# Optimization experiments

Hardware: AMD Instinct MI355X
Metric: run time of the kernel (lower is better)

The kernel has to match this reference:

```python
import jax, jax.numpy as jnp
import numpy as np
from jax import lax

B, T, D, H, L = 2048, 512, 64, 16, 10
LOG2PI = float(np.log(2.0 * np.pi))


def _gru_cell(x, h, Wih, Whh, bih, bhh):
    # torch GRUCell gate order: r, z, n
    gi = x @ Wih.T + bih
    gh = h @ Whh.T + bhh
    ir, iz, inn = jnp.split(gi, 3, axis=-1)
    hr, hz, hn = jnp.split(gh, 3, axis=-1)
    r = jax.nn.sigmoid(ir + hr)
    z = jax.nn.sigmoid(iz + hz)
    n = jnp.tanh(inn + r * hn)
    return (1.0 - z) * n + z * h


def _mlp_head(h, W1, b1, W2, b2, Wmu, bmu, Wcov, bcov):
    hh = jax.nn.relu(h @ W1.T + b1)
    hh = jax.nn.relu(hh @ W2.T + b2)
    mu = hh @ Wmu.T + bmu
    sigma = jnp.exp(hh @ Wcov.T + bcov)
    return mu, sigma


def setup_inputs():
    key = jax.random.key(0)
    ks = jax.random.split(key, 24)

    def he(k, shape, fan_in):
        return jax.random.normal(k, shape, dtype=jnp.float32) * np.float32(np.sqrt(2.0 / fan_in))

    z = lambda *s: jnp.zeros(s, jnp.float32)
    p = {}
    p['x'] = jax.random.normal(ks[0], (B, T, D), dtype=jnp.float32)
    p['eps'] = jax.random.normal(ks[1], (B, T, L), dtype=jnp.float32)
    # bidirectional inference GRU
    p['bi_Wih_f'] = he(ks[2], (3 * H, D), D); p['bi_Whh_f'] = he(ks[3], (3 * H, H), H)
    p['bi_bih_f'] = z(3 * H); p['bi_bhh_f'] = z(3 * H)
    p['bi_Wih_b'] = he(ks[4], (3 * H, D), D); p['bi_Whh_b'] = he(ks[5], (3 * H, H), H)
    p['bi_bih_b'] = z(3 * H); p['bi_bhh_b'] = z(3 * H)
    # inference GRUCell on [z_prev, context]
    p['infz_Wih'] = he(ks[6], (3 * H, L + 2 * H), L + 2 * H); p['infz_Whh'] = he(ks[7], (3 * H, H), H)
    p['infz_bih'] = z(3 * H); p['infz_bhh'] = z(3 * H)
    # inference MLP
    p['inf_W1'] = he(ks[8], (H, H), H); p['inf_b1'] = z(H)
    p['inf_W2'] = he(ks[9], (H, H), H); p['inf_b2'] = z(H)
    p['inf_Wmu'] = he(ks[10], (L, H), H); p['inf_bmu'] = z(L)
    p['inf_Wcov'] = he(ks[11], (L, H), H); p['inf_bcov'] = z(L)
    # generative prior GRUCell + MLP (frozen in torch)
    p['genz_Wih'] = he(ks[12], (3 * H, L), L); p['genz_Whh'] = he(ks[13], (3 * H, H), H)
    p['genz_bih'] = z(3 * H); p['genz_bhh'] = z(3 * H)
    p['genzmlp_W1'] = he(ks[14], (H, H), H); p['genzmlp_b1'] = z(H)
    p['genzmlp_W2'] = he(ks[15], (H, H), H); p['genzmlp_b2'] = z(H)
    p['genzmlp_Wmu'] = he(ks[16], (L, H), H); p['genzmlp_bmu'] = z(L)
    p['genzmlp_Wcov'] = he(ks[17], (L, H), H); p['genzmlp_bcov'] = z(L)
    # generative emission GRUCell + MLP (outputs 3*D)
    p['genr_Wih'] = he(ks[18], (3 * H, L), L); p['genr_Whh'] = he(ks[19], (3 * H, H), H)
    p['genr_bih'] = z(3 * H); p['genr_bhh'] = z(3 * H)
    p['genr_W1'] = he(ks[20], (H, H), H); p['genr_b1'] = z(H)
    p['genr_W2'] = he(ks[21], (3 * D, H), H); p['genr_b2'] = z(3 * D)
    return p


def _forward(x, eps, bi_Wih_f, bi_Whh_f, bi_bih_f, bi_bhh_f, bi_Wih_b, bi_Whh_b, bi_bih_b, bi_bhh_b,
             infz_Wih, infz_Whh, infz_bih, infz_bhh,
             inf_W1, inf_b1, inf_W2, inf_b2, inf_Wmu, inf_bmu, inf_Wcov, inf_bcov,
             genz_Wih, genz_Whh, genz_bih, genz_bhh,
             genzmlp_W1, genzmlp_b1, genzmlp_W2, genzmlp_b2, genzmlp_Wmu, genzmlp_bmu, genzmlp_Wcov, genzmlp_bcov,
             genr_Wih, genr_Whh, genr_bih, genr_bhh, genr_W1, genr_b1, genr_W2, genr_b2):
    b, t, d = x.shape
    xt = jnp.transpose(x, (1, 0, 2))      # [T, B, D] time-major
    eps_t = jnp.transpose(eps, (1, 0, 2))  # [T, B, L]
    h0 = jnp.zeros((b, H), x.dtype)

    def fstep(h, xin):
        h2 = _gru_cell(xin, h, bi_Wih_f, bi_Whh_f, bi_bih_f, bi_bhh_f)
        return h2, h2

    def bstep(h, xin):
        h2 = _gru_cell(xin, h, bi_Wih_b, bi_Whh_b, bi_bih_b, bi_bhh_b)
        return h2, h2

    _, fwd = lax.scan(fstep, h0, xt)               # [T, B, H]
    _, bwd_rev = lax.scan(bstep, h0, xt[::-1])
    bwd = bwd_rev[::-1]                            # [T, B, H]

    pad = jnp.zeros((1, b, H), x.dtype)
    h_right = jnp.concatenate([pad, fwd[:-1]], axis=0)   # h^{->}_{t-1}
    h_left = jnp.concatenate([bwd[1:], pad], axis=0)     # h^{<-}_{t+1}
    ctx = jnp.concatenate([h_right, h_left], axis=-1)    # [T, B, 2H]

    def step(carry, inp):
        h_z, h_gz, h_gr, z_prev = carry
        c, e, xi = inp
        h_z = _gru_cell(jnp.concatenate([z_prev, c], axis=-1), h_z, infz_Wih, infz_Whh, infz_bih, infz_bhh)
        q_mu, q_sig = _mlp_head(h_z, inf_W1, inf_b1, inf_W2, inf_b2, inf_Wmu, inf_bmu, inf_Wcov, inf_bcov)
        h_gz = _gru_cell(z_prev, h_gz, genz_Wih, genz_Whh, genz_bih, genz_bhh)
        p_mu, p_sig = _mlp_head(h_gz, genzmlp_W1, genzmlp_b1, genzmlp_W2, genzmlp_b2, genzmlp_Wmu, genzmlp_bmu, genzmlp_Wcov, genzmlp_bcov)
        # KL(N(q_mu,q_sig) || N(p_mu,p_sig))
        kl = jnp.log(p_sig / q_sig) + (q_sig * q_sig + (q_mu - p_mu) ** 2) / (2.0 * p_sig * p_sig) - 0.5
        kl_t = kl.sum(axis=-1).mean()
        z_t = q_mu + q_sig * e  # rsample
        h_gr = _gru_cell(z_t, h_gr, genr_Wih, genr_Whh, genr_bih, genr_bhh)
        r = jax.nn.relu(h_gr @ genr_W1.T + genr_b1) @ genr_W2.T + genr_b2  # [B, 3D]
        r_mu = r[:, :d]
        r_diag = jnp.exp(r[:, d:2 * d]) + 1e-4
        w = r[:, 2 * d:]  # rank-1 cov factor
        # LowRankMVN log_prob via Woodbury (rank 1): Cov = D + w w^T
        delta = xi - r_mu
        dinv = 1.0 / r_diag
        wd = w * dinv
        cap = 1.0 + jnp.sum(wd * w, axis=-1)  # capacitance
        maha = jnp.sum(delta * delta * dinv, axis=-1) - jnp.sum(wd * delta, axis=-1) ** 2 / cap
        logdet = jnp.sum(jnp.log(r_diag), axis=-1) + jnp.log(cap)
        logp = -0.5 * (d * LOG2PI + logdet + maha)
        nll_t = -logp.mean()
        return (h_z, h_gz, h_gr, z_t), (kl_t, nll_t)

    z0 = jnp.zeros((b, L), x.dtype)
    carry0 = (h0, h0, h0, z0)
    _, (kls, nlls) = lax.scan(step, carry0, (ctx, eps_t, xt))
    return nlls.sum(), kls.sum()


def reference(x, eps, bi_Wih_f, bi_Whh_f, bi_bih_f, bi_bhh_f, bi_Wih_b, bi_Whh_b, bi_bih_b, bi_bhh_b,
              infz_Wih, infz_Whh, infz_bih, infz_bhh,
              inf_W1, inf_b1, inf_W2, inf_b2, inf_Wmu, inf_bmu, inf_Wcov, inf_bcov,
              genz_Wih, genz_Whh, genz_bih, genz_bhh,
              genzmlp_W1, genzmlp_b1, genzmlp_W2, genzmlp_b2, genzmlp_Wmu, genzmlp_bmu, genzmlp_Wcov, genzmlp_bcov,
              genr_Wih, genr_Whh, genr_bih, genr_bhh, genr_W1, genr_b1, genr_W2, genr_b2):
    return _forward(x, eps, bi_Wih_f, bi_Whh_f, bi_bih_f, bi_bhh_f, bi_Wih_b, bi_Whh_b, bi_bih_b, bi_bhh_b,
                    infz_Wih, infz_Whh, infz_bih, infz_bhh,
                    inf_W1, inf_b1, inf_W2, inf_b2, inf_Wmu, inf_bmu, inf_Wcov, inf_bcov,
                    genz_Wih, genz_Whh, genz_bih, genz_bhh,
                    genzmlp_W1, genzmlp_b1, genzmlp_W2, genzmlp_b2, genzmlp_Wmu, genzmlp_bmu, genzmlp_Wcov, genzmlp_bcov,
                    genr_Wih, genr_Whh, genr_bih, genr_bhh, genr_W1, genr_b1, genr_W2, genr_b2)
```

## Files before the change

kernel.cpp:

```cpp
#include <hip/hip_runtime.h>

namespace {

typedef __attribute__((ext_vector_type(4))) _Float16 half4v;
typedef __attribute__((ext_vector_type(4))) float   float4v;
typedef unsigned int u32;

#define MFMA16(a,b,c) __builtin_amdgcn_mfma_f32_16x16x16f16((a),(b),(c),0,0,0)

constexpr int Bb = 2048;
constexpr int Tt = 512;
constexpr float LOG2PI_ = 1.8378770664093453f;

struct InPtrs { const float* p[42]; };

__device__ __forceinline__ float rcpf(float x){ return __builtin_amdgcn_rcpf(x); }
__device__ __forceinline__ float sigm(float x){ return rcpf(1.0f + __expf(-x)); }
__device__ __forceinline__ float tanh_(float x){ return 1.0f - 2.0f*rcpf(1.0f + __expf(2.0f*x)); }

__device__ __forceinline__ void barrier_lds(){
  asm volatile("s_waitcnt lgkmcnt(0)" ::: "memory");
  __builtin_amdgcn_s_barrier();
  asm volatile("" ::: "memory");
}

__global__ void zero2(float* out){ if (threadIdx.x < 2) out[threadIdx.x] = 0.f; }

__device__ __forceinline__ void gru_update(const float4v& Dr, const float4v& Dz,
                                           const float4v& Dn, const float4v& Dh, half4v& hB){
  #pragma unroll
  for (int i = 0; i < 4; ++i){
    const float rr = sigm(Dr[i]);
    const float zz = sigm(Dz[i]);
    const float nn = tanh_(Dn[i] + rr*Dh[i]);
    const float hp = (float)hB[i];
    hB[i] = (_Float16)(nn + zz*(hp - nn));
  }
}

__device__ __forceinline__ half4v relu_pack(const float4v& D){
  half4v o;
  #pragma unroll
  for (int i = 0; i < 4; ++i) o[i] = (_Float16)fmaxf(D[i], 0.f);
  return o;
}

constexpr int CH = 8;
constexpr int NCH = Tt / CH;

__global__ __launch_bounds__(128,1) void bigru(InPtrs ip, _Float16* __restrict__ hf,
                                               _Float16* __restrict__ hb)
{
  const int tid = threadIdx.x;
  const int w = tid >> 6;
  const int l = tid & 63, r = l & 15, q = l >> 4;
  const int dir = blockIdx.y;
  const int base = blockIdx.x * 16;

  const float* __restrict__ x   = ip.p[0];
  const float* __restrict__ Wih = dir ? ip.p[6] : ip.p[2];
  const float* __restrict__ Whh = dir ? ip.p[7] : ip.p[3];
  const float* __restrict__ bih = dir ? ip.p[8] : ip.p[4];
  const float* __restrict__ bhh = dir ? ip.p[9] : ip.p[5];
  _Float16* __restrict__ hout = dir ? hb : hf;

  __shared__ __align__(16) float giS[2][CH][64][12];

  half4v Wi[3][4];
  float  b0[4], b1[4], b2[4];
  float4v xp[CH][4];
  half4v Wh[3];
  float  bh2[4];
  half4v hB = {0,0,0,0};
  const float* xrow = x + (size_t)(base + r) * Tt * 64;

  if (w == 1){
    #pragma unroll
    for (int rt = 0; rt < 3; ++rt)
      #pragma unroll
      for (int kt = 0; kt < 4; ++kt)
        #pragma unroll
        for (int j = 0; j < 4; ++j)
          Wi[rt][kt][j] = (_Float16)Wih[(rt*16 + r)*64 + kt*16 + q*4 + j];
    #pragma unroll
    for (int i = 0; i < 4; ++i){
      const int row = q*4 + i;
      b0[i] = bih[row]      + bhh[row];
      b1[i] = bih[16 + row] + bhh[16 + row];
      b2[i] = bih[32 + row];
    }
    #pragma unroll
    for (int s = 0; s < CH; ++s){
      const int tn = dir ? Tt-1-s : s;
      #pragma unroll
      for (int kt = 0; kt < 4; ++kt)
        xp[s][kt] = *(const float4v*)(xrow + (size_t)tn*64 + kt*16 + q*4);
    }
  } else {
    #pragma unroll
    for (int rt = 0; rt < 3; ++rt)
      #pragma unroll
      for (int j = 0; j < 4; ++j)
        Wh[rt][j] = (_Float16)Whh[(rt*16 + r)*16 + q*4 + j];
    #pragma unroll
    for (int i = 0; i < 4; ++i) bh2[i] = bhh[32 + q*4 + i];
  }

  for (int c = 0; c < NCH; ++c){
    if (w == 1){
      #pragma unroll
      for (int st = 0; st < CH; ++st){
        const int tg = c*CH + st;
        half4v xB[4];
        #pragma unroll
        for (int kt = 0; kt < 4; ++kt)
          #pragma unroll
          for (int j = 0; j < 4; ++j) xB[kt][j] = (_Float16)xp[st][kt][j];
        const int tp = tg + CH;
        if (tp < Tt){
          const int tn = dir ? Tt-1-tp : tp;
          #pragma unroll
          for (int kt = 0; kt < 4; ++kt)
            xp[st][kt] = *(const float4v*)(xrow + (size_t)tn*64 + kt*16 + q*4);
        }
        float4v A0 = {b0[0],b0[1],b0[2],b0[3]};
        float4v A1 = {b1[0],b1[1],b1[2],b1[3]};
        float4v A2 = {b2[0],b2[1],b2[2],b2[3]};
        #pragma unroll
        for (int kt = 0; kt < 4; ++kt){
          A0 = MFMA16(Wi[0][kt], xB[kt], A0);
          A1 = MFMA16(Wi[1][kt], xB[kt], A1);
          A2 = MFMA16(Wi[2][kt], xB[kt], A2);
        }
        float* o = &giS[c&1][st][l][0];
        *(float4v*)(o + 0) = A0;
        *(float4v*)(o + 4) = A1;
        *(float4v*)(o + 8) = A2;
      }
    }
    barrier_lds();
    if (w == 0){
      #pragma unroll
      for (int st = 0; st < CH; ++st){
        const int tg = c*CH + st;
        const int t = dir ? Tt-1-tg : tg;
        const float* gi = &giS[c&1][st][l][0];
        float4v A0 = *(const float4v*)(gi + 0);
        float4v A1 = *(const float4v*)(gi + 4);
        float4v A2 = *(const float4v*)(gi + 8);
        float4v Dh = {bh2[0],bh2[1],bh2[2],bh2[3]};
        A0 = MFMA16(Wh[0], hB, A0);
        A1 = MFMA16(Wh[1], hB, A1);
        Dh = MFMA16(Wh[2], hB, Dh);
        gru_update(A0, A1, A2, Dh, hB);
        *(half4v*)(hout + (((size_t)t*Bb + base + r) << 4) + q*4) = hB;
      }
    }
  }
}

__global__ __launch_bounds__(192,1) void vae_seq(InPtrs ip, const _Float16* __restrict__ hf,
                                                 const _Float16* __restrict__ hb,
                                                 _Float16* __restrict__ hz,
                                                 _Float16* __restrict__ hgz,
                                                 _Float16* __restrict__ hgr)
{
  const int tid = threadIdx.x;
  const int w = tid / 64;
  const int l = tid & 63, r = l & 15, q = l >> 4;
  const int base = blockIdx.x * 16;
  const int row0 = q*4;

  __shared__ u32 zS[3][2][64];
  for (int i = tid; i < 3*2*64; i += 192) ((u32*)zS)[i] = 0u;
  barrier_lds();

  half4v WizA[3][3], WhzA[3], I1A, I2A, IMuA, ICovA;
  float bz0[4], bz1[4], bzn[4], bzh[4], bI1v[4], bI2v[4], bIMu[4], bICov[4];
  half4v hzB = {0,0,0,0}, zB = {0,0,0,0};
  half4v hrR[4], hlR[4];
  float4v eR[4];
  half4v WgzA[3], WhgzA[3];
  float bg0[4], bg1[4], bgn[4], bgh[4];
  half4v hgzB = {0,0,0,0};
  half4v WgrA[3], WhgrA[3];
  float br0[4], br1[4], brn[4], brh[4];
  half4v hgrB = {0,0,0,0};

  const float* erow = ip.p[1] + (size_t)(base + r) * Tt * 10;

  if (w == 0){
    #pragma unroll
    for (int rt = 0; rt < 3; ++rt)
      #pragma unroll
      for (int kt = 0; kt < 3; ++kt)
        #pragma unroll
        for (int j = 0; j < 4; ++j){
          const int k = kt*16 + q*4 + j;
          int c;
          if (kt == 0) c = (k < 10) ? k : -1;
          else if (kt == 1) c = 10 + (k - 16);
          else c = 26 + (k - 32);
          WizA[rt][kt][j] = (c >= 0) ? (_Float16)ip.p[10][(rt*16 + r)*42 + c] : (_Float16)0.f;
        }
    #pragma unroll
    for (int rt = 0; rt < 3; ++rt)
      #pragma unroll
      for (int j = 0; j < 4; ++j)
        WhzA[rt][j] = (_Float16)ip.p[11][(rt*16 + r)*16 + q*4 + j];
    #pragma unroll
    for (int j = 0; j < 4; ++j){
      const int k = q*4 + j;
      I1A[j]  = (_Float16)ip.p[14][r*16 + k];
      I2A[j]  = (_Float16)ip.p[16][r*16 + k];
      IMuA[j] = (r < 10) ? (_Float16)ip.p[18][r*16 + k] : (_Float16)0.f;
      ICovA[j]= (r < 10) ? (_Float16)ip.p[20][r*16 + k] : (_Float16)0.f;
    }
    #pragma unroll
    for (int i = 0; i < 4; ++i){
      const int row = row0 + i;
      bz0[i] = ip.p[12][row]    + ip.p[13][row];
      bz1[i] = ip.p[12][16+row] + ip.p[13][16+row];
      bzn[i] = ip.p[12][32+row];
      bzh[i] = ip.p[13][32+row];
      bI1v[i] = ip.p[15][row];  bI2v[i] = ip.p[17][row];
      bIMu[i]  = (row < 10) ? ip.p[19][row] : 0.f;
      bICov[i] = (row < 10) ? ip.p[21][row] : 0.f;
    }
    #pragma unroll
    for (int s = 0; s < 4; ++s){
      if (s >= 1) hrR[s] = *(const half4v*)(hf + (((size_t)(s-1)*Bb + base + r) << 4) + q*4);
      else { half4v z0 = {0,0,0,0}; hrR[s] = z0; }
      hlR[s] = *(const half4v*)(hb + (((size_t)(s+1)*Bb + base + r) << 4) + q*4);
      float4v et;
      #pragma unroll
      for (int ii = 0; ii < 4; ++ii) et[ii] = (row0 + ii < 10) ? erow[s*10 + row0 + ii] : 0.f;
      eR[s] = et;
    }
  } else if (w == 1){
    #pragma unroll
    for (int rt = 0; rt < 3; ++rt)
      #pragma unroll
      for (int j = 0; j < 4; ++j){
        const int k = q*4 + j;
        WgzA[rt][j]  = (k < 10) ? (_Float16)ip.p[22][(rt*16 + r)*10 + k] : (_Float16)0.f;
        WhgzA[rt][j] = (_Float16)ip.p[23][(rt*16 + r)*16 + k];
      }
    #pragma unroll
    for (int i = 0; i < 4; ++i){
      const int row = row0 + i;
      bg0[i] = ip.p[24][row]    + ip.p[25][row];
      bg1[i] = ip.p[24][16+row] + ip.p[25][16+row];
      bgn[i] = ip.p[24][32+row];
      bgh[i] = ip.p[25][32+row];
    }
  } else {
    #pragma unroll
    for (int rt = 0; rt < 3; ++rt)
      #pragma unroll
      for (int j = 0; j < 4; ++j){
        const int k = q*4 + j;
        WgrA[rt][j]  = (k < 10) ? (_Float16)ip.p[34][(rt*16 + r)*10 + k] : (_Float16)0.f;
        WhgrA[rt][j] = (_Float16)ip.p[35][(rt*16 + r)*16 + k];
      }
    #pragma unroll
    for (int i = 0; i < 4; ++i){
      const int row = row0 + i;
      br0[i] = ip.p[36][row]    + ip.p[37][row];
      br1[i] = ip.p[36][16+row] + ip.p[37][16+row];
      brn[i] = ip.p[36][32+row];
      brh[i] = ip.p[37][32+row];
    }
  }

  for (int ib = 0; ib < Tt + 4; ib += 4){
    #pragma unroll
    for (int k = 0; k < 4; ++k){
      const int i = ib + k;
      if (w == 0){
        if (i < Tt){
          const half4v hrB = hrR[k], hlB = hlR[k];
          const float4v ev = eR[k];
          const int f = i + 4;
          if (f < Tt){
            hrR[k] = *(const half4v*)(hf + (((size_t)(f-1)*Bb + base + r) << 4) + q*4);
            if (f <= Tt-2) hlR[k] = *(const half4v*)(hb + (((size_t)(f+1)*Bb + base + r) << 4) + q*4);
            else { half4v z0 = {0,0,0,0}; hlR[k] = z0; }
            float4v et;
            #pragma unroll
            for (int ii = 0; ii < 4; ++ii) et[ii] = (row0 + ii < 10) ? erow[f*10 + row0 + ii] : 0.f;
            eR[k] = et;
          }
          float4v Dr = {bz0[0],bz0[1],bz0[2],bz0[3]};
          float4v Dz = {bz1[0],bz1[1],bz1[2],bz1[3]};
          float4v Dn = {bzn[0],bzn[1],bzn[2],bzn[3]};
          float4v Dh = {bzh[0],bzh[1],bzh[2],bzh[3]};
          Dr = MFMA16(WizA[0][1], hrB, Dr); Dr = MFMA16(WizA[0][2], hlB, Dr);
          Dz = MFMA16(WizA[1][1], hrB, Dz); Dz = MFMA16(WizA[1][2], hlB, Dz);
          Dn = MFMA16(WizA[2][1], hrB, Dn); Dn = MFMA16(WizA[2][2], hlB, Dn);
          Dr = MFMA16(WhzA[0], hzB, Dr);
          Dz = MFMA16(WhzA[1], hzB, Dz);
          Dh = MFMA16(WhzA[2], hzB, Dh);
          Dr = MFMA16(WizA[0][0], zB, Dr);
          Dz = MFMA16(WizA[1][0], zB, Dz);
          Dn = MFMA16(WizA[2][0], zB, Dn);
          gru_update(Dr, Dz, Dn, Dh, hzB);
          *(half4v*)(hz + (((size_t)i*Bb + base + r) << 4) + q*4) = hzB;

          float4v H1 = {bI1v[0],bI1v[1],bI1v[2],bI1v[3]};
          H1 = MFMA16(I1A, hzB, H1);
          const half4v h1B = relu_pack(H1);
          float4v H2 = {bI2v[0],bI2v[1],bI2v[2],bI2v[3]};
          H2 = MFMA16(I2A, h1B, H2);
          const half4v h2B = relu_pack(H2);
          float4v Qmu  = {bIMu[0],bIMu[1],bIMu[2],bIMu[3]};
          float4v Qpre = {bICov[0],bICov[1],bICov[2],bICov[3]};
          Qmu  = MFMA16(IMuA,  h2B, Qmu);
          Qpre = MFMA16(ICovA, h2B, Qpre);

          const int slot = i % 3;
          #pragma unroll
          for (int ii = 0; ii < 4; ++ii){
            const float qs = __expf(Qpre[ii]);
            zB[ii] = (_Float16)(Qmu[ii] + qs*ev[ii]);
          }
          union { half4v h; u32 u[2]; } zc; zc.h = zB;
          zS[slot][0][l] = zc.u[0];
          zS[slot][1][l] = zc.u[1];
        }
      } else if (w == 1){
        if (i >= 1 && i <= Tt){
          const int s = i - 1;
          const int sp = (s - 1 + 3) % 3;
          union { half4v h; u32 u[2]; } zc;
          zc.u[0] = zS[sp][0][l]; zc.u[1] = zS[sp][1][l];
          const half4v zPrev = zc.h;

          float4v Er = {bg0[0],bg0[1],bg0[2],bg0[3]};
          float4v Ez = {bg1[0],bg1[1],bg1[2],bg1[3]};
          float4v En = {bgn[0],bgn[1],bgn[2],bgn[3]};
          float4v Eh = {bgh[0],bgh[1],bgh[2],bgh[3]};
          Er = MFMA16(WgzA[0], zPrev, Er); Er = MFMA16(WhgzA[0], hgzB, Er);
          Ez = MFMA16(WgzA[1], zPrev, Ez); Ez = MFMA16(WhgzA[1], hgzB, Ez);
          En = MFMA16(WgzA[2], zPrev, En);
          Eh = MFMA16(WhgzA[2], hgzB, Eh);
          gru_update(Er, Ez, En, Eh, hgzB);
          *(half4v*)(hgz + (((size_t)s*Bb + base + r) << 4) + q*4) = hgzB;
        }
      } else {
        if (i >= 2 && i < Tt + 2){
          const int u = i - 2;
          union { half4v h; u32 uu[2]; } zc;
          zc.uu[0] = zS[u % 3][0][l]; zc.uu[1] = zS[u % 3][1][l];
          const half4v zU = zc.h;

          float4v Fr = {br0[0],br0[1],br0[2],br0[3]};
          float4v Fz = {br1[0],br1[1],br1[2],br1[3]};
          float4v Fn = {brn[0],brn[1],brn[2],brn[3]};
          float4v Fh = {brh[0],brh[1],brh[2],brh[3]};
          Fr = MFMA16(WgrA[0], zU, Fr); Fr = MFMA16(WhgrA[0], hgrB, Fr);
          Fz = MFMA16(WgrA[1], zU, Fz); Fz = MFMA16(WhgrA[1], hgrB, Fz);
          Fn = MFMA16(WgrA[2], zU, Fn);
          Fh = MFMA16(WhgrA[2], hgrB, Fh);
          gru_update(Fr, Fz, Fn, Fh, hgrB);
          *(half4v*)(hgr + (((size_t)u*Bb + base + r) << 4) + q*4) = hgrB;
        }
      }
      barrier_lds();
    }
  }
}

__global__ __launch_bounds__(256,2) void epi(InPtrs ip, const _Float16* __restrict__ hz,
                                             const _Float16* __restrict__ hgz,
                                             const _Float16* __restrict__ hgr,
                                             float* __restrict__ out)
{
  const int tid = threadIdx.x;
  const int l = tid & 63, r = l & 15, q = l >> 4;
  const int row0 = q*4;

  if (blockIdx.x < 1024){
    const int wid = blockIdx.x * 4 + (tid >> 6);
    const int u0 = wid * 16;

    half4v I1A, I2A, IMuA, ICovA, Z1A, Z2A, ZMuA, ZCovA;
    float bI1v[4], bI2v[4], bIMu[4], bICov[4], bZ1v[4], bZ2v[4], bZMu[4], bZCov[4];
    #pragma unroll
    for (int j = 0; j < 4; ++j){
      const int k = q*4 + j;
      I1A[j]  = (_Float16)ip.p[14][r*16 + k];
      I2A[j]  = (_Float16)ip.p[16][r*16 + k];
      IMuA[j] = (r < 10) ? (_Float16)ip.p[18][r*16 + k] : (_Float16)0.f;
      ICovA[j]= (r < 10) ? (_Float16)ip.p[20][r*16 + k] : (_Float16)0.f;
      Z1A[j]  = (_Float16)ip.p[26][r*16 + k];
      Z2A[j]  = (_Float16)ip.p[28][r*16 + k];
      ZMuA[j] = (r < 10) ? (_Float16)ip.p[30][r*16 + k] : (_Float16)0.f;
      ZCovA[j]= (r < 10) ? (_Float16)ip.p[32][r*16 + k] : (_Float16)0.f;
    }
    #pragma unroll
    for (int i = 0; i < 4; ++i){
      const int row = row0 + i;
      bI1v[i] = ip.p[15][row];  bI2v[i] = ip.p[17][row];
      bIMu[i]  = (row < 10) ? ip.p[19][row] : 0.f;
      bICov[i] = (row < 10) ? ip.p[21][row] : 0.f;
      bZ1v[i] = ip.p[27][row];  bZ2v[i] = ip.p[29][row];
      bZMu[i]  = (row < 10) ? ip.p[31][row] : 0.f;
      bZCov[i] = (row < 10) ? ip.p[33][row] : 0.f;
    }

    float kl_acc = 0.f;
    for (int k = 0; k < 16; ++k){
      const int u = u0 + k;
      const int tile = u >> 9, t = u & 511;
      const size_t off = (((size_t)t*Bb + tile*16 + r) << 4) + q*4;
      const half4v hzB  = *(const half4v*)(hz  + off);
      const half4v hgzB = *(const half4v*)(hgz + off);

      float4v H1 = {bI1v[0],bI1v[1],bI1v[2],bI1v[3]};
      H1 = MFMA16(I1A, hzB, H1);
      const half4v h1B = relu_pack(H1);
      float4v H2 = {bI2v[0],bI2v[1],bI2v[2],bI2v[3]};
      H2 = MFMA16(I2A, h1B, H2);
      const half4v h2B = relu_pack(H2);
      float4v Qmu  = {bIMu[0],bIMu[1],bIMu[2],bIMu[3]};
      float4v Qpre = {bICov[0],bICov[1],bICov[2],bICov[3]};
      Qmu  = MFMA16(IMuA,  h2B, Qmu);
      Qpre = MFMA16(ICovA, h2B, Qpre);

      float4v G1 = {bZ1v[0],bZ1v[1],bZ1v[2],bZ1v[3]};
      G1 = MFMA16(Z1A, hgzB, G1);
      const half4v g1B = relu_pack(G1);
      float4v G2 = {bZ2v[0],bZ2v[1],bZ2v[2],bZ2v[3]};
      G2 = MFMA16(Z2A, g1B, G2);
      const half4v g2B = relu_pack(G2);
      float4v Pmu  = {bZMu[0],bZMu[1],bZMu[2],bZMu[3]};
      float4v Ppre = {bZCov[0],bZCov[1],bZCov[2],bZCov[3]};
      Pmu  = MFMA16(ZMuA,  g2B, Pmu);
      Ppre = MFMA16(ZCovA, g2B, Ppre);

      #pragma unroll
      for (int ii = 0; ii < 4; ++ii){
        const float qs = __expf(Qpre[ii]);
        const float dm = Qmu[ii] - Pmu[ii];
        kl_acc += (Ppre[ii] - Qpre[ii]) + (qs*qs + dm*dm)*0.5f*__expf(-2.f*Ppre[ii]) - 0.5f;
      }
    }
    #pragma unroll
    for (int m = 1; m < 64; m <<= 1) kl_acc += __shfl_xor(kl_acc, m, 64);
    if (l == 0) atomicAdd(&out[1], kl_acc * (1.f/(float)Bb));
  } else {
    const int wid = (blockIdx.x - 1024) * 4 + (tid >> 6);
    const int u0 = wid * 16;

    half4v R1A, R2A[12];
    float bR1v[4], bR2v[12][4];
    #pragma unroll
    for (int j = 0; j < 4; ++j){
      const int k = q*4 + j;
      R1A[j] = (_Float16)ip.p[38][r*16 + k];
      #pragma unroll
      for (int m = 0; m < 12; ++m)
        R2A[m][j] = (_Float16)ip.p[40][(m*16 + r)*16 + k];
    }
    #pragma unroll
    for (int i = 0; i < 4; ++i){
      const int row = row0 + i;
      bR1v[i] = ip.p[39][row];
      #pragma unroll
      for (int m = 0; m < 12; ++m) bR2v[m][i] = ip.p[41][m*16 + row];
    }

    float nll_acc = 0.f;
    for (int k = 0; k < 16; ++k){
      const int u = u0 + k;
      const int tile = u >> 9, t = u & 511;
      const half4v hgrB = *(const half4v*)(hgr + (((size_t)t*Bb + tile*16 + r) << 4) + q*4);
      const float* xrow = ip.p[0] + ((size_t)(tile*16 + r) * Tt + t) * 64;
      float4v xv[4];
      #pragma unroll
      for (int m = 0; m < 4; ++m) xv[m] = *(const float4v*)(xrow + m*16 + q*4);

      float4v R1D = {bR1v[0],bR1v[1],bR1v[2],bR1v[3]};
      R1D = MFMA16(R1A, hgrB, R1D);
      const half4v r1B = relu_pack(R1D);

      float s1 = 0.f, s2 = 0.f, s3 = 0.f, s4 = 0.f;
      #pragma unroll
      for (int m = 0; m < 4; ++m){
        float4v Dmu = {bR2v[m][0],bR2v[m][1],bR2v[m][2],bR2v[m][3]};
        float4v Ddp = {bR2v[4+m][0],bR2v[4+m][1],bR2v[4+m][2],bR2v[4+m][3]};
        float4v Dw  = {bR2v[8+m][0],bR2v[8+m][1],bR2v[8+m][2],bR2v[8+m][3]};
        Dmu = MFMA16(R2A[m],   r1B, Dmu);
        Ddp = MFMA16(R2A[4+m], r1B, Ddp);
        Dw  = MFMA16(R2A[8+m], r1B, Dw);
        #pragma unroll
        for (int ii = 0; ii < 4; ++ii){
          const float diag = __expf(Ddp[ii]) + 1e-4f;
          const float dinv = rcpf(diag);
          const float delta = xv[m][ii] - Dmu[ii];
          const float wv = Dw[ii];
          s1 += delta*delta*dinv;
          s2 += wv*wv*dinv;
          s3 += wv*dinv*delta;
          s4 += __logf(diag);
        }
      }
      s1 += __shfl_xor(s1, 16, 64); s1 += __shfl_xor(s1, 32, 64);
      s2 += __shfl_xor(s2, 16, 64); s2 += __shfl_xor(s2, 32, 64);
      s3 += __shfl_xor(s3, 16, 64); s3 += __shfl_xor(s3, 32, 64);
      s4 += __shfl_xor(s4, 16, 64); s4 += __shfl_xor(s4, 32, 64);
      const float cap = 1.f + s2;
      const float maha = s1 - s3*s3*rcpf(cap);
      const float logdet = s4 + __logf(cap);
      nll_acc += 0.5f*(64.f*LOG2PI_ + logdet + maha);
    }
    #pragma unroll
    for (int m = 1; m < 64; m <<= 1) nll_acc += __shfl_xor(nll_acc, m, 64);
    if (l == 0) atomicAdd(&out[0], nll_acc * 0.25f * (1.f/(float)Bb));
  }
}

}

extern "C" void kernel_launch(void* const* d_in, const int* in_sizes, int n_in,
                              void* d_out, int out_size, void* d_ws, size_t ws_size,
                              hipStream_t stream)
{
  InPtrs ip;
  for (int i = 0; i < 42; ++i) ip.p[i] = (const float*)d_in[i];
  float* out = (float*)d_out;

  const size_t SZ = (size_t)Tt * Bb * 16;
  _Float16* hf  = (_Float16*)d_ws;
  _Float16* hb  = hf  + SZ;
  _Float16* hz  = hb  + SZ;
  _Float16* hgz = hz  + SZ;
  _Float16* hgr = hgz + SZ;

  zero2<<<1, 64, 0, stream>>>(out);
  dim3 gb(Bb/16, 2);
  bigru<<<gb, 128, 0, stream>>>(ip, hf, hb);
  vae_seq<<<Bb/16, 192, 0, stream>>>(ip, hf, hb, hz, hgz, hgr);
  epi<<<2048, 256, 0, stream>>>(ip, hz, hgz, hgr, out);
}
```

Before: 1.029 ms.

## Halve barriers in wavefront-pipelined VAE sequence via deeper z ring buffer

The z ring buffer shared between the three wave roles grows from 3 to 8 slots, and the downstream waves now lag by 2 and 4 steps instead of 1 and 2. This lets the loop skip the LDS barrier on every other iteration, cutting barrier stalls on the serial time loop. Separately, the float atomics into the output are replaced by per-block partial sums plus a final single-block reduction kernel, which also removes the zeroing kernel. The deeper lag adds a few pipeline drain steps, and correctness relies on the slot and lag arithmetic staying race-free with half the barriers.

Result: faster. 996.9 us (-3.1%).

```diff
diff --git a/kernel.cpp b/kernel.cpp
--- a/kernel.cpp
+++ b/kernel.cpp
@@ -23,8 +23,6 @@
   __builtin_amdgcn_s_barrier();
   asm volatile("" ::: "memory");
 }
-
-__global__ void zero2(float* out){ if (threadIdx.x < 2) out[threadIdx.x] = 0.f; }
 
 __device__ __forceinline__ void gru_update(const float4v& Dr, const float4v& Dz,
                                            const float4v& Dn, const float4v& Dh, half4v& hB){
@@ -171,8 +169,8 @@
   const int base = blockIdx.x * 16;
   const int row0 = q*4;
 
-  __shared__ u32 zS[3][2][64];
-  for (int i = tid; i < 3*2*64; i += 192) ((u32*)zS)[i] = 0u;
+  __shared__ u32 zS[8][2][64];
+  for (int i = tid; i < 8*2*64; i += 192) ((u32*)zS)[i] = 0u;
   barrier_lds();
 
   half4v WizA[3][3], WhzA[3], I1A, I2A, IMuA, ICovA;
@@ -318,21 +316,21 @@
           Qmu  = MFMA16(IMuA,  h2B, Qmu);
           Qpre = MFMA16(ICovA, h2B, Qpre);
 
-          const int slot = i % 3;
           #pragma unroll
           for (int ii = 0; ii < 4; ++ii){
             const float qs = __expf(Qpre[ii]);
             zB[ii] = (_Float16)(Qmu[ii] + qs*ev[ii]);
           }
           union { half4v h; u32 u[2]; } zc; zc.h = zB;
+          const int slot = i & 7;
           zS[slot][0][l] = zc.u[0];
           zS[slot][1][l] = zc.u[1];
         }
       } else if (w == 1){
-        if (i >= 1 && i <= Tt){
-          const int s = i - 1;
-          const int sp = (s - 1 + 3) % 3;
+        if (i >= 2 && i < Tt + 2){
+          const int s = i - 2;
           union { half4v h; u32 u[2]; } zc;
+          const int sp = (s - 1) & 7;
           zc.u[0] = zS[sp][0][l]; zc.u[1] = zS[sp][1][l];
           const half4v zPrev = zc.h;
 
@@ -348,10 +346,11 @@
           *(half4v*)(hgz + (((size_t)s*Bb + base + r) << 4) + q*4) = hgzB;
         }
       } else {
-        if (i >= 2 && i < Tt + 2){
-          const int u = i - 2;
+        if (i >= 4 && i < Tt + 4){
+          const int u = i - 4;
           union { half4v h; u32 uu[2]; } zc;
-          zc.uu[0] = zS[u % 3][0][l]; zc.uu[1] = zS[u % 3][1][l];
+          const int su = u & 7;
+          zc.uu[0] = zS[su][0][l]; zc.uu[1] = zS[su][1][l];
           const half4v zU = zc.h;
 
           float4v Fr = {br0[0],br0[1],br0[2],br0[3]};
@@ -366,7 +365,7 @@
           *(half4v*)(hgr + (((size_t)u*Bb + base + r) << 4) + q*4) = hgrB;
         }
       }
-      barrier_lds();
+      if (k & 1) barrier_lds();
     }
   }
 }
@@ -374,11 +373,12 @@
 __global__ __launch_bounds__(256,2) void epi(InPtrs ip, const _Float16* __restrict__ hz,
                                              const _Float16* __restrict__ hgz,
                                              const _Float16* __restrict__ hgr,
-                                             float* __restrict__ out)
+                                             float* __restrict__ red)
 {
   const int tid = threadIdx.x;
   const int l = tid & 63, r = l & 15, q = l >> 4;
   const int row0 = q*4;
+  __shared__ float sred[4];
 
   if (blockIdx.x < 1024){
     const int wid = blockIdx.x * 4 + (tid >> 6);
@@ -448,7 +448,9 @@
     }
     #pragma unroll
     for (int m = 1; m < 64; m <<= 1) kl_acc += __shfl_xor(kl_acc, m, 64);
-    if (l == 0) atomicAdd(&out[1], kl_acc * (1.f/(float)Bb));
+    if (l == 0) sred[tid >> 6] = kl_acc;
+    __syncthreads();
+    if (tid == 0) red[blockIdx.x] = sred[0] + sred[1] + sred[2] + sred[3];
   } else {
     const int wid = (blockIdx.x - 1024) * 4 + (tid >> 6);
     const int u0 = wid * 16;
@@ -517,7 +519,32 @@
     }
     #pragma unroll
     for (int m = 1; m < 64; m <<= 1) nll_acc += __shfl_xor(nll_acc, m, 64);
-    if (l == 0) atomicAdd(&out[0], nll_acc * 0.25f * (1.f/(float)Bb));
+    if (l == 0) sred[tid >> 6] = nll_acc;
+    __syncthreads();
+    if (tid == 0) red[blockIdx.x] = sred[0] + sred[1] + sred[2] + sred[3];
+  }
+}
+
+__global__ __launch_bounds__(256,1) void finred(const float* __restrict__ red,
+                                                float* __restrict__ out)
+{
+  const int tid = threadIdx.x;
+  float a = 0.f, b = 0.f;
+  for (int i = tid; i < 1024; i += 256){
+    a += red[i];
+    b += red[1024 + i];
+  }
+  #pragma unroll
+  for (int m = 1; m < 64; m <<= 1){
+    a += __shfl_xor(a, m, 64);
+    b += __shfl_xor(b, m, 64);
+  }
+  __shared__ float sa[4], sb[4];
+  if ((tid & 63) == 0){ sa[tid >> 6] = a; sb[tid >> 6] = b; }
+  __syncthreads();
+  if (tid == 0){
+    out[1] = (sa[0] + sa[1] + sa[2] + sa[3]) * (1.f/(float)Bb);
+    out[0] = (sb[0] + sb[1] + sb[2] + sb[3]) * 0.25f * (1.f/(float)Bb);
   }
 }
 
@@ -537,10 +564,11 @@
   _Float16* hz  = hb  + SZ;
   _Float16* hgz = hz  + SZ;
   _Float16* hgr = hgz + SZ;
-
-  zero2<<<1, 64, 0, stream>>>(out);
+  float* red    = (float*)(hgr + SZ);
+
   dim3 gb(Bb/16, 2);
   bigru<<<gb, 128, 0, stream>>>(ip, hf, hb);
   vae_seq<<<Bb/16, 192, 0, stream>>>(ip, hf, hb, hz, hgz, hgr);
-  epi<<<2048, 256, 0, stream>>>(ip, hz, hgz, hgr, out);
-}
+  epi<<<2048, 256, 0, stream>>>(ip, hz, hgz, hgr, red);
+  finred<<<1, 256, 0, stream>>>(red, out);
+}
```
